# Performance work log

Measured on AMD Instinct MI355X. Metric: run time of the kernel, lower is better.

The kernel has to match this reference:

```python
import jax, jax.numpy as jnp
import numpy as np

B, T, MAX_ITEMS = 128, 50, 32
NUM_PRODUCT, E, EW = 100000, 128, 16
D = E + EW  # rnn input/hidden size


def setup_inputs() -> dict:
    key = jax.random.key(0)
    ks = jax.random.split(key, 10)
    # items: 0 is padding; keep roughly half the slots padded (ragged baskets)
    items = jax.random.randint(ks[0], (B, T, MAX_ITEMS), 1, NUM_PRODUCT)
    keep = jax.random.uniform(ks[1], (B, T, MAX_ITEMS)) < 0.5
    keep = keep.at[:, :, 0].set(True)  # at least one item per basket
    items = jnp.where(keep, items, 0)
    flag = jax.random.randint(ks[2], (B, T, 1), 0, 2)
    x = jnp.concatenate([items, flag], axis=-1)  # [B,T,MAX_ITEMS+1], last col = flag
    lengths = jnp.full((B,), T, dtype=jnp.int64)
    hidden = jnp.zeros((1, B, D), dtype=jnp.float32)
    s_e = 1.0 / np.sqrt(E)
    s_d = 1.0 / np.sqrt(D)
    encode_w = jax.random.uniform(ks[3], (NUM_PRODUCT, E), minval=-0.1, maxval=0.1)
    encode_w = encode_w.at[0].set(0.0)  # padding_idx=0
    wchange_w = jax.random.normal(ks[4], (2, EW)) * 0.1
    wchange_w = wchange_w.at[0].set(0.0)  # padding_idx=0
    w_ih = jax.random.uniform(ks[5], (3 * D, D), minval=-s_d, maxval=s_d)
    w_hh = jax.random.uniform(ks[6], (3 * D, D), minval=-s_d, maxval=s_d)
    b_ih = jax.random.uniform(ks[7], (3 * D,), minval=-s_d, maxval=s_d)
    b_hh = jax.random.uniform(ks[8], (3 * D,), minval=-s_d, maxval=s_d)
    fc_w = jax.random.uniform(ks[9], (E, D), minval=-s_d, maxval=s_d)
    fc_b = jnp.zeros((E,), dtype=jnp.float32)
    return {"x": x, "lengths": lengths, "hidden": hidden,
            "encode_w": encode_w, "wchange_w": wchange_w,
            "w_ih": w_ih, "w_hh": w_hh, "b_ih": b_ih, "b_hh": b_hh,
            "fc_w": fc_w, "fc_b": fc_b}


def _embed_baskets(x, encode_w, wchange_w):
    items = x[..., :-1]                      # [B,T,I] product ids, 0 = pad
    flag = x[..., -1]                        # [B,T] 0/1 weight-change flag
    emb = encode_w[items]                    # [B,T,I,E] fused ragged gather
    mask = (items != 0).astype(emb.dtype)[..., None]
    cnt = jnp.maximum(mask.sum(axis=2), 1.0)
    pooled = (emb * mask).sum(axis=2) / cnt  # avg pool over real items [B,T,E]
    w = wchange_w[flag]                      # [B,T,EW]
    return jnp.concatenate([pooled, w], axis=-1)  # [B,T,D]


def _gru(seq, h0, w_ih, w_hh, b_ih, b_hh):
    # seq: [B,T,D], h0: [B,D]; torch GRU cell math
    def step(h, x_t):
        gi = x_t @ w_ih.T + b_ih             # [B,3D]
        gh = h @ w_hh.T + b_hh
        i_r, i_z, i_n = jnp.split(gi, 3, axis=-1)
        h_r, h_z, h_n = jnp.split(gh, 3, axis=-1)
        r = jax.nn.sigmoid(i_r + h_r)
        z = jax.nn.sigmoid(i_z + h_z)
        n = jnp.tanh(i_n + r * h_n)
        h_new = (1.0 - z) * n + z * h
        return h_new, h_new
    h_last, outs = jax.lax.scan(step, h0, jnp.swapaxes(seq, 0, 1))
    return jnp.swapaxes(outs, 0, 1), h_last  # [B,T,D], [B,D]


def reference(x, lengths, hidden, encode_w, wchange_w, w_ih, w_hh, b_ih, b_hh, fc_w, fc_b):
    seq = _embed_baskets(x, encode_w, wchange_w)         # [B,T,D]
    out, h_last = _gru(seq, hidden[0], w_ih, w_hh, b_ih, b_hh)
    dynamic_user = out @ fc_w.T + fc_b                   # [B,T,E]
    return dynamic_user, h_last[None]                    # h_u: [1,B,D]
```

## Files before the change

### kernel.cpp

```cpp
#include <hip/hip_runtime.h>
#include <math.h>

#define B_   128
#define T_   50
#define MI_  32
#define E_   128
#define EW_  16
#define D_   144
#define G_   432
#define N_   (B_*T_)

__global__ __launch_bounds__(256) void embed_kernel(
    const int* __restrict__ x,
    const float* __restrict__ encode_w,
    const float* __restrict__ wchange_w,
    float* __restrict__ seq)
{
    int n = blockIdx.x;
    int tid = threadIdx.x;
    int i = tid >> 3;
    int j = tid & 7;

    __shared__ int xi[33];
    __shared__ __align__(16) float part[32 * 132];
    __shared__ float cntf[32];

    if (tid < 33) xi[tid] = x[n * 33 + tid];
    __syncthreads();

    int it = xi[i];
    const float* row = &encode_w[(size_t)it * E_];
    float4 v0 = *(const float4*)&row[16 * j + 0];
    float4 v1 = *(const float4*)&row[16 * j + 4];
    float4 v2 = *(const float4*)&row[16 * j + 8];
    float4 v3 = *(const float4*)&row[16 * j + 12];

    float* p = &part[i * 132 + 16 * j];
    *(float4*)&p[0]  = v0;
    *(float4*)&p[4]  = v1;
    *(float4*)&p[8]  = v2;
    *(float4*)&p[12] = v3;
    if (j == 0) cntf[i] = (it != 0) ? 1.f : 0.f;
    __syncthreads();

    if (tid < E_) {
        int c = tid;
        float s = 0.f, cn = 0.f;
        #pragma unroll
        for (int k = 0; k < 32; ++k) {
            s  += part[k * 132 + c];
            cn += cntf[k];
        }
        seq[n * D_ + c] = s / fmaxf(cn, 1.f);
    } else if (tid < E_ + EW_) {
        int c = tid - E_;
        seq[n * D_ + E_ + c] = wchange_w[xi[32] * EW_ + c];
    }
}

template<int CTRL>
__device__ __forceinline__ float dpp_xor_add(float x) {
    int y = __builtin_amdgcn_mov_dpp(__float_as_int(x), CTRL, 0xF, 0xF, true);
    return x + __int_as_float(y);
}
#define DPP_RED3(v) \
    v = dpp_xor_add<0xB1>(v); v = dpp_xor_add<0x4E>(v); v = dpp_xor_add<0x141>(v);

__global__ __launch_bounds__(576) void gi_matvec_kernel(
    const float* __restrict__ seq,
    const float* __restrict__ w_ih,
    const float* __restrict__ b_ih,
    float* __restrict__ gi)
{
    int n0 = blockIdx.x * 25;
    int tid = threadIdx.x;
    int g = tid >> 3;
    int s = tid & 7;
    int k0 = s * 20;

    __shared__ __align__(16) float sq[25 * 160];

    {
        float4* d4 = (float4*)sq;
        const float4* s4 = (const float4*)(seq + (size_t)n0 * D_);
        for (int idx = tid; idx < 100; idx += 576) {
            int i = idx >> 2, p = idx & 3;
            d4[i * 40 + 36 + p] = make_float4(0.f, 0.f, 0.f, 0.f);
        }
        for (int idx = tid; idx < 900; idx += 576) {
            int i = idx / 36, q = idx - i * 36;
            d4[i * 40 + q] = s4[i * 36 + q];
        }
    }

    float w[6][20];
    #pragma unroll
    for (int r = 0; r < 6; ++r) {
        const float* wrow = &w_ih[(size_t)(6 * g + r) * D_];
        #pragma unroll
        for (int q = 0; q < 5; ++q) {
            int k = k0 + 4 * q;
            float4 t = make_float4(0.f, 0.f, 0.f, 0.f);
            if (k < D_) t = *(const float4*)&wrow[k];
            w[r][4 * q + 0] = t.x;
            w[r][4 * q + 1] = t.y;
            w[r][4 * q + 2] = t.z;
            w[r][4 * q + 3] = t.w;
        }
    }
    float bias = (s < 6) ? b_ih[6 * g + s] : 0.f;
    __syncthreads();

    const float* hp = sq + k0;
    float* gp = gi + (size_t)n0 * G_ + 6 * g + s;
    for (int i = 0; i < 25; ++i) {
        float hv[20];
        #pragma unroll
        for (int q = 0; q < 5; ++q) {
            float4 t4 = *(const float4*)&hp[i * 160 + 4 * q];
            hv[4 * q + 0] = t4.x;
            hv[4 * q + 1] = t4.y;
            hv[4 * q + 2] = t4.z;
            hv[4 * q + 3] = t4.w;
        }
        float a0 = 0.f, a1 = 0.f, a2 = 0.f, a3 = 0.f, a4 = 0.f, a5 = 0.f;
        #pragma unroll
        for (int kk = 0; kk < 20; ++kk) {
            float hk = hv[kk];
            a0 = fmaf(w[0][kk], hk, a0);
            a1 = fmaf(w[1][kk], hk, a1);
            a2 = fmaf(w[2][kk], hk, a2);
            a3 = fmaf(w[3][kk], hk, a3);
            a4 = fmaf(w[4][kk], hk, a4);
            a5 = fmaf(w[5][kk], hk, a5);
        }
        DPP_RED3(a0); DPP_RED3(a1); DPP_RED3(a2);
        DPP_RED3(a3); DPP_RED3(a4); DPP_RED3(a5);
        float myacc = a0;
        if (s == 1) myacc = a1;
        if (s == 2) myacc = a2;
        if (s == 3) myacc = a3;
        if (s == 4) myacc = a4;
        if (s == 5) myacc = a5;
        if (s < 6) gp[(size_t)i * G_] = myacc + bias;
    }
}

__global__ __launch_bounds__(512) void fc_matvec_kernel(
    const float* __restrict__ hseq,
    const float* __restrict__ fc_w,
    const float* __restrict__ fc_b,
    float* __restrict__ dyn)
{
    int n0 = blockIdx.x * 25;
    int tid = threadIdx.x;
    int g = tid >> 3;
    int s = tid & 7;
    int k0 = s * 20;

    __shared__ __align__(16) float sq[25 * 160];

    {
        float4* d4 = (float4*)sq;
        const float4* s4 = (const float4*)(hseq + (size_t)n0 * D_);
        for (int idx = tid; idx < 100; idx += 512) {
            int i = idx >> 2, p = idx & 3;
            d4[i * 40 + 36 + p] = make_float4(0.f, 0.f, 0.f, 0.f);
        }
        for (int idx = tid; idx < 900; idx += 512) {
            int i = idx / 36, q = idx - i * 36;
            d4[i * 40 + q] = s4[i * 36 + q];
        }
    }

    float w[2][20];
    #pragma unroll
    for (int r = 0; r < 2; ++r) {
        const float* wrow = &fc_w[(size_t)(2 * g + r) * D_];
        #pragma unroll
        for (int q = 0; q < 5; ++q) {
            int k = k0 + 4 * q;
            float4 t = make_float4(0.f, 0.f, 0.f, 0.f);
            if (k < D_) t = *(const float4*)&wrow[k];
            w[r][4 * q + 0] = t.x;
            w[r][4 * q + 1] = t.y;
            w[r][4 * q + 2] = t.z;
            w[r][4 * q + 3] = t.w;
        }
    }
    float bias = (s < 2) ? fc_b[2 * g + s] : 0.f;
    __syncthreads();

    const float* hp = sq + k0;
    float* gp = dyn + (size_t)n0 * E_ + 2 * g + s;
    for (int i = 0; i < 25; ++i) {
        float hv[20];
        #pragma unroll
        for (int q = 0; q < 5; ++q) {
            float4 t4 = *(const float4*)&hp[i * 160 + 4 * q];
            hv[4 * q + 0] = t4.x;
            hv[4 * q + 1] = t4.y;
            hv[4 * q + 2] = t4.z;
            hv[4 * q + 3] = t4.w;
        }
        float f0 = 0.f, f1 = 0.f;
        #pragma unroll
        for (int kk = 0; kk < 20; ++kk) {
            float hk = hv[kk];
            f0 = fmaf(w[0][kk], hk, f0);
            f1 = fmaf(w[1][kk], hk, f1);
        }
        DPP_RED3(f0); DPP_RED3(f1);
        float myacc = (s == 0) ? f0 : f1;
        if (s < 2) gp[(size_t)i * E_] = myacc + bias;
    }
}

__global__ __launch_bounds__(576) void gru_kernel(
    const float* __restrict__ gi,
    const float* __restrict__ w_hh,
    const float* __restrict__ b_hh,
    const float* __restrict__ h0,
    float* __restrict__ hseq,
    float* __restrict__ hlast)
{
    int b = blockIdx.x;
    int tid = threadIdx.x;
    int g = tid >> 3;
    int s = tid & 7;
    int k0 = s * 20;

    __shared__ __align__(16) float h[160];
    __shared__ float gh[G_];

    float w[6][20];
    #pragma unroll
    for (int r = 0; r < 6; ++r) {
        const float* wrow = &w_hh[(size_t)(6 * g + r) * D_];
        #pragma unroll
        for (int q = 0; q < 5; ++q) {
            int k = k0 + 4 * q;
            float4 t = make_float4(0.f, 0.f, 0.f, 0.f);
            if (k < D_) t = *(const float4*)&wrow[k];
            w[r][4 * q + 0] = t.x;
            w[r][4 * q + 1] = t.y;
            w[r][4 * q + 2] = t.z;
            w[r][4 * q + 3] = t.w;
        }
    }
    float bias = (s < 6) ? b_hh[6 * g + s] : 0.f;

    if (tid < 160) h[tid] = (tid < D_) ? h0[b * D_ + tid] : 0.f;
    __syncthreads();

    float gir = 0.f, giz = 0.f, gin = 0.f;
    if (tid < D_) {
        const float* gp = &gi[(size_t)(b * T_) * G_];
        gir = gp[tid];
        giz = gp[D_ + tid];
        gin = gp[2 * D_ + tid];
    }

    for (int t = 0; t < T_; ++t) {
        int n = b * T_ + t;

        float girU = gir, gizU = giz, ginU = gin;
        if (tid < D_ && t + 1 < T_) {
            const float* gp = &gi[(size_t)(n + 1) * G_];
            gir = gp[tid];
            giz = gp[D_ + tid];
            gin = gp[2 * D_ + tid];
        }

        float hv[20];
        #pragma unroll
        for (int q = 0; q < 5; ++q) {
            float4 t4 = *(const float4*)&h[k0 + 4 * q];
            hv[4 * q + 0] = t4.x;
            hv[4 * q + 1] = t4.y;
            hv[4 * q + 2] = t4.z;
            hv[4 * q + 3] = t4.w;
        }

        float a0 = 0.f, a1 = 0.f, a2 = 0.f, a3 = 0.f, a4 = 0.f, a5 = 0.f;
        #pragma unroll
        for (int kk = 0; kk < 20; ++kk) {
            float hk = hv[kk];
            a0 = fmaf(w[0][kk], hk, a0);
            a1 = fmaf(w[1][kk], hk, a1);
            a2 = fmaf(w[2][kk], hk, a2);
            a3 = fmaf(w[3][kk], hk, a3);
            a4 = fmaf(w[4][kk], hk, a4);
            a5 = fmaf(w[5][kk], hk, a5);
        }

        DPP_RED3(a0); DPP_RED3(a1); DPP_RED3(a2);
        DPP_RED3(a3); DPP_RED3(a4); DPP_RED3(a5);

        float myacc = a0;
        if (s == 1) myacc = a1;
        if (s == 2) myacc = a2;
        if (s == 3) myacc = a3;
        if (s == 4) myacc = a4;
        if (s == 5) myacc = a5;
        if (s < 6) gh[6 * g + s] = myacc + bias;
        __syncthreads();

        if (tid < D_) {
            float r = 1.f / (1.f + __expf(-(girU + gh[tid])));
            float z = 1.f / (1.f + __expf(-(gizU + gh[D_ + tid])));
            float narg = ginU + r * gh[2 * D_ + tid];
            narg = fminf(fmaxf(narg, -15.f), 15.f);
            float e2 = __expf(-2.f * narg);
            float nn = (1.f - e2) / (1.f + e2);
            float hn = (1.f - z) * nn + z * h[tid];
            hseq[(size_t)n * D_ + tid] = hn;
            h[tid] = hn;
        }
        __syncthreads();
    }

    if (tid < D_) hlast[b * D_ + tid] = h[tid];
}

extern "C" void kernel_launch(void* const* d_in, const int* in_sizes, int n_in,
                              void* d_out, int out_size, void* d_ws, size_t ws_size,
                              hipStream_t stream)
{
    const int*   x         = (const int*)d_in[0];
    const float* hidden    = (const float*)d_in[2];
    const float* encode_w  = (const float*)d_in[3];
    const float* wchange_w = (const float*)d_in[4];
    const float* w_ih      = (const float*)d_in[5];
    const float* w_hh      = (const float*)d_in[6];
    const float* b_ih      = (const float*)d_in[7];
    const float* b_hh      = (const float*)d_in[8];
    const float* fc_w      = (const float*)d_in[9];
    const float* fc_b      = (const float*)d_in[10];

    float* out = (float*)d_out;
    float* ws  = (float*)d_ws;
    float* seq  = ws;
    float* gi   = ws + 921600;
    float* hseq = ws + 921600 + 2764800;

    embed_kernel<<<N_, 256, 0, stream>>>(x, encode_w, wchange_w, seq);

    gi_matvec_kernel<<<256, 576, 0, stream>>>(seq, w_ih, b_ih, gi);

    gru_kernel<<<B_, 576, 0, stream>>>(gi, w_hh, b_hh, hidden, hseq,
                                       out + (size_t)N_ * E_);

    fc_matvec_kernel<<<256, 512, 0, stream>>>(hseq, fc_w, fc_b, out);
}
```

Measured before the change: 193.5 us.

## Fuse embedding into input projection and FC into GRU kernel

Merges the basket embedding/pooling into the input-gate matvec kernel so pooled rows go straight to shared memory instead of a global seq buffer. The GRU kernel also keeps its hidden states in shared memory and runs the output FC projection itself, dropping the hseq buffer and two launches. The cost is that the embedding gathers now run serially per timestep inside 256 blocks, with two barriers each, instead of across thousands of blocks. The FC also becomes a serial tail on only 128 blocks.

```diff
diff --git a/kernel.cpp b/kernel.cpp
--- a/kernel.cpp
+++ b/kernel.cpp
@@ -10,54 +10,6 @@
 #define G_   432
 #define N_   (B_*T_)
 
-__global__ __launch_bounds__(256) void embed_kernel(
-    const int* __restrict__ x,
-    const float* __restrict__ encode_w,
-    const float* __restrict__ wchange_w,
-    float* __restrict__ seq)
-{
-    int n = blockIdx.x;
-    int tid = threadIdx.x;
-    int i = tid >> 3;
-    int j = tid & 7;
-
-    __shared__ int xi[33];
-    __shared__ __align__(16) float part[32 * 132];
-    __shared__ float cntf[32];
-
-    if (tid < 33) xi[tid] = x[n * 33 + tid];
-    __syncthreads();
-
-    int it = xi[i];
-    const float* row = &encode_w[(size_t)it * E_];
-    float4 v0 = *(const float4*)&row[16 * j + 0];
-    float4 v1 = *(const float4*)&row[16 * j + 4];
-    float4 v2 = *(const float4*)&row[16 * j + 8];
-    float4 v3 = *(const float4*)&row[16 * j + 12];
-
-    float* p = &part[i * 132 + 16 * j];
-    *(float4*)&p[0]  = v0;
-    *(float4*)&p[4]  = v1;
-    *(float4*)&p[8]  = v2;
-    *(float4*)&p[12] = v3;
-    if (j == 0) cntf[i] = (it != 0) ? 1.f : 0.f;
-    __syncthreads();
-
-    if (tid < E_) {
-        int c = tid;
-        float s = 0.f, cn = 0.f;
-        #pragma unroll
-        for (int k = 0; k < 32; ++k) {
-            s  += part[k * 132 + c];
-            cn += cntf[k];
-        }
-        seq[n * D_ + c] = s / fmaxf(cn, 1.f);
-    } else if (tid < E_ + EW_) {
-        int c = tid - E_;
-        seq[n * D_ + E_ + c] = wchange_w[xi[32] * EW_ + c];
-    }
-}
-
 template<int CTRL>
 __device__ __forceinline__ float dpp_xor_add(float x) {
     int y = __builtin_amdgcn_mov_dpp(__float_as_int(x), CTRL, 0xF, 0xF, true);
@@ -66,32 +18,62 @@
 #define DPP_RED3(v) \
     v = dpp_xor_add<0xB1>(v); v = dpp_xor_add<0x4E>(v); v = dpp_xor_add<0x141>(v);
 
-__global__ __launch_bounds__(576) void gi_matvec_kernel(
-    const float* __restrict__ seq,
+__global__ __launch_bounds__(576) void embed_gi_kernel(
+    const int* __restrict__ x,
+    const float* __restrict__ encode_w,
+    const float* __restrict__ wchange_w,
     const float* __restrict__ w_ih,
     const float* __restrict__ b_ih,
     float* __restrict__ gi)
 {
     int n0 = blockIdx.x * 25;
     int tid = threadIdx.x;
+
+    __shared__ int xiAll[25 * 33];
+    __shared__ __align__(16) float part[32 * 132];
+    __shared__ float cntf[32];
+    __shared__ __align__(16) float sq[25 * 160];
+
+    for (int idx = tid; idx < 25 * 33; idx += 576)
+        xiAll[idx] = x[(size_t)n0 * 33 + idx];
+    for (int idx = tid; idx < 25 * 16; idx += 576) {
+        int i = idx >> 4, c = idx & 15;
+        sq[i * 160 + 144 + c] = 0.f;
+    }
+    __syncthreads();
+
+    int it_i = tid >> 4;
+    int it_j = tid & 15;
+    for (int i = 0; i < 25; ++i) {
+        if (tid < 512) {
+            int it = xiAll[i * 33 + it_i];
+            const float* row = &encode_w[(size_t)it * E_];
+            float4 v0 = *(const float4*)&row[8 * it_j + 0];
+            float4 v1 = *(const float4*)&row[8 * it_j + 4];
+            float* p = &part[it_i * 132 + 8 * it_j];
+            *(float4*)&p[0] = v0;
+            *(float4*)&p[4] = v1;
+            if (it_j == 0) cntf[it_i] = (it != 0) ? 1.f : 0.f;
+        }
+        __syncthreads();
+        if (tid < E_) {
+            float s = 0.f, cn = 0.f;
+            #pragma unroll
+            for (int k = 0; k < 32; ++k) {
+                s  += part[k * 132 + tid];
+                cn += cntf[k];
+            }
+            sq[i * 160 + tid] = s / fmaxf(cn, 1.f);
+        } else if (tid < E_ + EW_) {
+            int c = tid - E_;
+            sq[i * 160 + E_ + c] = wchange_w[xiAll[i * 33 + 32] * EW_ + c];
+        }
+        __syncthreads();
+    }
+
     int g = tid >> 3;
     int s = tid & 7;
     int k0 = s * 20;
-
-    __shared__ __align__(16) float sq[25 * 160];
-
-    {
-        float4* d4 = (float4*)sq;
-        const float4* s4 = (const float4*)(seq + (size_t)n0 * D_);
-        for (int idx = tid; idx < 100; idx += 576) {
-            int i = idx >> 2, p = idx & 3;
-            d4[i * 40 + 36 + p] = make_float4(0.f, 0.f, 0.f, 0.f);
-        }
-        for (int idx = tid; idx < 900; idx += 576) {
-            int i = idx / 36, q = idx - i * 36;
-            d4[i * 40 + q] = s4[i * 36 + q];
-        }
-    }
 
     float w[6][20];
     #pragma unroll
@@ -109,7 +91,6 @@
         }
     }
     float bias = (s < 6) ? b_ih[6 * g + s] : 0.f;
-    __syncthreads();
 
     const float* hp = sq + k0;
     float* gp = gi + (size_t)n0 * G_ + 6 * g + s;
@@ -146,37 +127,30 @@
     }
 }
 
-__global__ __launch_bounds__(512) void fc_matvec_kernel(
-    const float* __restrict__ hseq,
+__global__ __launch_bounds__(576) void gru_fc_kernel(
+    const float* __restrict__ gi,
+    const float* __restrict__ w_hh,
+    const float* __restrict__ b_hh,
+    const float* __restrict__ h0,
     const float* __restrict__ fc_w,
     const float* __restrict__ fc_b,
-    float* __restrict__ dyn)
+    float* __restrict__ dyn,
+    float* __restrict__ hlast)
 {
-    int n0 = blockIdx.x * 25;
+    int b = blockIdx.x;
     int tid = threadIdx.x;
     int g = tid >> 3;
     int s = tid & 7;
     int k0 = s * 20;
 
-    __shared__ __align__(16) float sq[25 * 160];
-
-    {
-        float4* d4 = (float4*)sq;
-        const float4* s4 = (const float4*)(hseq + (size_t)n0 * D_);
-        for (int idx = tid; idx < 100; idx += 512) {
-            int i = idx >> 2, p = idx & 3;
-            d4[i * 40 + 36 + p] = make_float4(0.f, 0.f, 0.f, 0.f);
-        }
-        for (int idx = tid; idx < 900; idx += 512) {
-            int i = idx / 36, q = idx - i * 36;
-            d4[i * 40 + q] = s4[i * 36 + q];
-        }
-    }
-
-    float w[2][20];
+    __shared__ __align__(16) float h[160];
+    __shared__ float gh[G_];
+    __shared__ __align__(16) float hcache[T_ * 160];
+
+    float w[6][20];
     #pragma unroll
-    for (int r = 0; r < 2; ++r) {
-        const float* wrow = &fc_w[(size_t)(2 * g + r) * D_];
+    for (int r = 0; r < 6; ++r) {
+        const float* wrow = &w_hh[(size_t)(6 * g + r) * D_];
         #pragma unroll
         for (int q = 0; q < 5; ++q) {
             int k = k0 + 4 * q;
@@ -188,69 +162,13 @@
             w[r][4 * q + 3] = t.w;
         }
     }
-    float bias = (s < 2) ? fc_b[2 * g + s] : 0.f;
-    __syncthreads();
-
-    const float* hp = sq + k0;
-    float* gp = dyn + (size_t)n0 * E_ + 2 * g + s;
-    for (int i = 0; i < 25; ++i) {
-        float hv[20];
-        #pragma unroll
-        for (int q = 0; q < 5; ++q) {
-            float4 t4 = *(const float4*)&hp[i * 160 + 4 * q];
-            hv[4 * q + 0] = t4.x;
-            hv[4 * q + 1] = t4.y;
-            hv[4 * q + 2] = t4.z;
-            hv[4 * q + 3] = t4.w;
-        }
-        float f0 = 0.f, f1 = 0.f;
-        #pragma unroll
-        for (int kk = 0; kk < 20; ++kk) {
-            float hk = hv[kk];
-            f0 = fmaf(w[0][kk], hk, f0);
-            f1 = fmaf(w[1][kk], hk, f1);
-        }
-        DPP_RED3(f0); DPP_RED3(f1);
-        float myacc = (s == 0) ? f0 : f1;
-        if (s < 2) gp[(size_t)i * E_] = myacc + bias;
-    }
-}
-
-__global__ __launch_bounds__(576) void gru_kernel(
-    const float* __restrict__ gi,
-    const float* __restrict__ w_hh,
-    const float* __restrict__ b_hh,
-    const float* __restrict__ h0,
-    float* __restrict__ hseq,
-    float* __restrict__ hlast)
-{
-    int b = blockIdx.x;
-    int tid = threadIdx.x;
-    int g = tid >> 3;
-    int s = tid & 7;
-    int k0 = s * 20;
-
-    __shared__ __align__(16) float h[160];
-    __shared__ float gh[G_];
-
-    float w[6][20];
-    #pragma unroll
-    for (int r = 0; r < 6; ++r) {
-        const float* wrow = &w_hh[(size_t)(6 * g + r) * D_];
-        #pragma unroll
-        for (int q = 0; q < 5; ++q) {
-            int k = k0 + 4 * q;
-            float4 t = make_float4(0.f, 0.f, 0.f, 0.f);
-            if (k < D_) t = *(const float4*)&wrow[k];
-            w[r][4 * q + 0] = t.x;
-            w[r][4 * q + 1] = t.y;
-            w[r][4 * q + 2] = t.z;
-            w[r][4 * q + 3] = t.w;
-        }
-    }
     float bias = (s < 6) ? b_hh[6 * g + s] : 0.f;
 
     if (tid < 160) h[tid] = (tid < D_) ? h0[b * D_ + tid] : 0.f;
+    for (int idx = tid; idx < T_ * 16; idx += 576) {
+        int i = idx >> 4, c = idx & 15;
+        hcache[i * 160 + 144 + c] = 0.f;
+    }
     __syncthreads();
 
     float gir = 0.f, giz = 0.f, gin = 0.f;
@@ -314,13 +232,55 @@
             float e2 = __expf(-2.f * narg);
             float nn = (1.f - e2) / (1.f + e2);
             float hn = (1.f - z) * nn + z * h[tid];
-            hseq[(size_t)n * D_ + tid] = hn;
+            hcache[t * 160 + tid] = hn;
             h[tid] = hn;
         }
         __syncthreads();
     }
 
     if (tid < D_) hlast[b * D_ + tid] = h[tid];
+
+    if (g < 64) {
+        float wf0[20], wf1[20];
+        #pragma unroll
+        for (int q = 0; q < 5; ++q) {
+            int k = k0 + 4 * q;
+            float4 t0 = make_float4(0.f, 0.f, 0.f, 0.f);
+            float4 t1 = t0;
+            if (k < D_) {
+                t0 = *(const float4*)&fc_w[(size_t)(2 * g + 0) * D_ + k];
+                t1 = *(const float4*)&fc_w[(size_t)(2 * g + 1) * D_ + k];
+            }
+            wf0[4 * q + 0] = t0.x; wf0[4 * q + 1] = t0.y;
+            wf0[4 * q + 2] = t0.z; wf0[4 * q + 3] = t0.w;
+            wf1[4 * q + 0] = t1.x; wf1[4 * q + 1] = t1.y;
+            wf1[4 * q + 2] = t1.z; wf1[4 * q + 3] = t1.w;
+        }
+        float fb = (s < 2) ? fc_b[2 * g + s] : 0.f;
+
+        const float* hp = hcache + k0;
+        float* dp = dyn + (size_t)(b * T_) * E_ + 2 * g + s;
+        for (int i = 0; i < T_; ++i) {
+            float hv[20];
+            #pragma unroll
+            for (int q = 0; q < 5; ++q) {
+                float4 t4 = *(const float4*)&hp[i * 160 + 4 * q];
+                hv[4 * q + 0] = t4.x;
+                hv[4 * q + 1] = t4.y;
+                hv[4 * q + 2] = t4.z;
+                hv[4 * q + 3] = t4.w;
+            }
+            float f0 = 0.f, f1 = 0.f;
+            #pragma unroll
+            for (int kk = 0; kk < 20; ++kk) {
+                float hk = hv[kk];
+                f0 = fmaf(wf0[kk], hk, f0);
+                f1 = fmaf(wf1[kk], hk, f1);
+            }
+            DPP_RED3(f0); DPP_RED3(f1);
+            if (s < 2) dp[(size_t)i * E_] = ((s == 0) ? f0 : f1) + fb;
+        }
+    }
 }
 
 extern "C" void kernel_launch(void* const* d_in, const int* in_sizes, int n_in,
@@ -339,17 +299,12 @@
     const float* fc_b      = (const float*)d_in[10];
 
     float* out = (float*)d_out;
-    float* ws  = (float*)d_ws;
-    float* seq  = ws;
-    float* gi   = ws + 921600;
-    float* hseq = ws + 921600 + 2764800;
-
-    embed_kernel<<<N_, 256, 0, stream>>>(x, encode_w, wchange_w, seq);
-
-    gi_matvec_kernel<<<256, 576, 0, stream>>>(seq, w_ih, b_ih, gi);
-
-    gru_kernel<<<B_, 576, 0, stream>>>(gi, w_hh, b_hh, hidden, hseq,
-                                       out + (size_t)N_ * E_);
-
-    fc_matvec_kernel<<<256, 512, 0, stream>>>(hseq, fc_w, fc_b, out);
+    float* gi  = (float*)d_ws;
+
+    embed_gi_kernel<<<256, 576, 0, stream>>>(x, encode_w, wchange_w,
+                                             w_ih, b_ih, gi);
+
+    gru_fc_kernel<<<B_, 576, 0, stream>>>(gi, w_hh, b_hh, hidden,
+                                          fc_w, fc_b,
+                                          out, out + (size_t)N_ * E_);
 }
```

Result: slower. 204.9 us (+5.9%).
